# Kernel optimization log

Hardware: AMD Instinct MI355X
Metric: run time of the kernel (lower is better)

The kernel has to match this reference:

```python
import jax, jax.numpy as jnp
import numpy as np

B, T, D, H, L = 8, 128, 400, 300, 45  # batch, max_length, 2*word_lstm_size, hidden, tag_count


def setup_inputs() -> dict:
    key = jax.random.key(0)
    ks = jax.random.split(key, 10)
    s = 0.05
    return {
        "cont_repr": jax.random.normal(ks[0], (B, T, D), jnp.float32),
        "root": jax.random.normal(ks[1], (1, 1, D), jnp.float32),
        "W1a": jax.random.normal(ks[2], (D, H), jnp.float32) * s,
        "W1b": jax.random.normal(ks[3], (D, H), jnp.float32) * s,
        "b1": jnp.zeros((H,), jnp.float32),
        "Wa": jax.random.normal(ks[4], (H, 1), jnp.float32) * s,
        "ba": jnp.zeros((1,), jnp.float32),
        "Wl": jax.random.normal(ks[5], (H, L), jnp.float32) * s,
        "bl": jnp.zeros((L,), jnp.float32),
        "sentence_lengths": jax.random.randint(ks[6], (B,), 0, T + 1),
        "desired_arcs": jax.random.randint(ks[7], (B, T), 0, T + 1),
        "desired_labels": jax.random.randint(ks[8], (B, T), 0, L),
        "use_desired_arcs": 1,
    }


def reference(cont_repr, root, W1a, W1b, b1, Wa, ba, Wl, bl,
              sentence_lengths, desired_arcs, desired_labels, use_desired_arcs):
    b, t, d = cont_repr.shape
    mask = (jnp.arange(t)[None, :] < sentence_lengths[:, None]).astype(cont_repr.dtype)  # [B,T]
    n_valid = jnp.maximum(mask.sum(), 1.0)

    # Dense(concat(tile_a, tile_b)) == tile_a @ W1a + tile_b @ W1b (exact same math,
    # avoids materializing the [B,T,T+1,2D] concat the TF graph builds).
    a_proj = jnp.einsum('btd,dh->bth', cont_repr, W1a)                     # [B,T,H]
    with_root = jnp.concatenate([jnp.broadcast_to(root, (b, 1, d)), cont_repr], axis=1)  # [B,T+1,D]
    b_proj = jnp.einsum('bsd,dh->bsh', with_root, W1b)                     # [B,T+1,H]
    h = jax.nn.relu(a_proj[:, :, None, :] + b_proj[:, None, :, :] + b1)    # [B,T,T+1,H]

    # UAS: arc scorer (units=1) over T+1 head candidates
    arc_logits = jnp.einsum('btsh,ho->btso', h, Wa)[..., 0] + ba[0]        # [B,T,T+1]
    predicted_arcs = jnp.argmax(arc_logits, axis=-1)                        # [B,T]
    arc_logp = jax.nn.log_softmax(arc_logits, axis=-1)
    arc_ce = -jnp.take_along_axis(arc_logp, desired_arcs[..., None], axis=-1)[..., 0]
    uas_loss = (arc_ce * mask).sum() / n_valid

    # LAS: gather pair repr at selected head, score labels
    sel = desired_arcs if use_desired_arcs else predicted_arcs             # [B,T]
    idx = jnp.broadcast_to(sel[:, :, None, None], (b, t, 1, h.shape[-1]))
    sel_h = jnp.take_along_axis(h, idx, axis=2)[:, :, 0, :]                # [B,T,H]
    lab_logits = jnp.einsum('bth,hl->btl', sel_h, Wl) + bl                 # [B,T,L]
    lab_logp = jax.nn.log_softmax(lab_logits, axis=-1)
    lab_ce = -jnp.take_along_axis(lab_logp, desired_labels[..., None], axis=-1)[..., 0]
    las_loss = (lab_ce * mask).sum() / n_valid

    return (uas_loss + las_loss) / 2
```

## Files before the change

### kernel.cpp

```cpp
#include <hip/hip_runtime.h>
#include <hip/hip_bf16.h>
#include <math.h>

#define BN 8
#define TT 128
#define DD 400
#define HH 300
#define LL 45
#define KH 200
#define SS 129
#define ALG_STRIDE 132

__global__ __launch_bounds__(640) void proj_kernel(
    const float* __restrict__ cont, const float* __restrict__ root,
    const float* __restrict__ W1a, const float* __restrict__ W1b,
    const float* __restrict__ b1,
    const int* __restrict__ slen,
    float* __restrict__ AP, float* __restrict__ BPX,
    float* __restrict__ accum)
{
    __shared__ float red[320][9];
    const int blk = blockIdx.x;
    const int tid = threadIdx.x;
    const int grp = tid / 320;
    const int h   = tid % 320;
    const int d0  = __builtin_amdgcn_readfirstlane(grp * KH);

    if (blk == 256) {
        if (tid == 0) accum[0] = 0.f;
        float acc = 0.f;
        if (h < HH) {
            const float* wp = W1b + (size_t)d0 * HH + h;
            for (int d = 0; d < KH; ++d)
                acc = fmaf(root[d0 + d], wp[(size_t)d * HH], acc);
        }
        if (grp == 1) red[h][0] = acc;
        __syncthreads();
        if (grp == 0 && h < HH) {
            const float v = acc + red[h][0];
            for (int bb = 0; bb < BN; ++bb)
                BPX[(size_t)bb * SS * HH + h] = v;
        }
        return;
    }

    const bool isA = (blk < 128);
    const int rb   = isA ? blk : blk - 128;
    const int row0 = rb * 8;
    if (isA) {
        const int lenb = slen[row0 >> 7];
        if ((row0 & 127) >= lenb) return;
    }

    const float* W    = isA ? W1a : W1b;
    const float* rows = cont + (size_t)row0 * DD + d0;

    float acc[8];
    #pragma unroll
    for (int r = 0; r < 8; ++r) acc[r] = 0.f;

    if (h < HH) {
        const float* wp = W + (size_t)d0 * HH + h;
        float w[8];
        #pragma unroll
        for (int k = 0; k < 8; ++k) w[k] = wp[(size_t)k * HH];
        for (int dc = 0; dc < KH; dc += 8) {
            float wn[8];
            if (dc + 8 < KH) {
                #pragma unroll
                for (int k = 0; k < 8; ++k) wn[k] = wp[(size_t)(dc + 8 + k) * HH];
            } else {
                #pragma unroll
                for (int k = 0; k < 8; ++k) wn[k] = 0.f;
            }
            #pragma unroll
            for (int r = 0; r < 8; ++r) {
                const float* rp = rows + r * DD + dc;
                #pragma unroll
                for (int k = 0; k < 8; ++k)
                    acc[r] = fmaf(rp[k], w[k], acc[r]);
            }
            #pragma unroll
            for (int k = 0; k < 8; ++k) w[k] = wn[k];
        }
    }

    if (grp == 1) {
        #pragma unroll
        for (int r = 0; r < 8; ++r) red[h][r] = acc[r];
    }
    __syncthreads();
    if (grp == 0 && h < HH) {
        if (isA) {
            const float bb = b1[h];
            float* dst = AP + (size_t)row0 * HH + h;
            #pragma unroll
            for (int r = 0; r < 8; ++r)
                dst[(size_t)r * HH] = acc[r] + red[h][r] + bb;
        } else {
            const int b = row0 >> 7, t = row0 & 127;
            float* dst = BPX + ((size_t)(b * SS + t + 1)) * HH + h;
            #pragma unroll
            for (int r = 0; r < 8; ++r)
                dst[(size_t)r * HH] = acc[r] + red[h][r];
        }
    }
}

__global__ __launch_bounds__(256) void arc_kernel(
    const float* __restrict__ AP, const float* __restrict__ BPX,
    const float* __restrict__ Wa, const int* __restrict__ slen,
    float* __restrict__ ALG)
{
    const int blk = blockIdx.x;
    const int b  = blk >> 8;
    const int tg = (blk >> 3) & 31;
    const int sc = blk & 7;
    const int t0 = tg * 4;
    if (t0 >= slen[b]) return;

    const int lane = threadIdx.x & 63;
    const int wave = threadIdx.x >> 6;

    const float* ap = AP + (size_t)(b * TT + t0) * HH;
    float apr[4][5], war[5];
    #pragma unroll
    for (int i = 0; i < 5; ++i) {
        const int hh = lane + 64 * i;
        const bool v = (hh < HH);
        war[i] = v ? Wa[hh] : 0.f;
        #pragma unroll
        for (int r = 0; r < 4; ++r)
            apr[r][i] = v ? ap[(size_t)r * HH + hh] : 0.f;
    }

    const int s0 = sc * 17;
    for (int sl = wave; sl < 17; sl += 4) {
        const int s = s0 + sl;
        if (s >= SS) break;
        const float* bp = BPX + (size_t)(b * SS + s) * HH;
        float bv[5];
        #pragma unroll
        for (int i = 0; i < 5; ++i) {
            const int hh = lane + 64 * i;
            bv[i] = (hh < HH) ? bp[hh] : 0.f;
        }
        float p0 = 0.f, p1 = 0.f, p2 = 0.f, p3 = 0.f;
        #pragma unroll
        for (int i = 0; i < 5; ++i) {
            p0 = fmaf(fmaxf(apr[0][i] + bv[i], 0.f), war[i], p0);
            p1 = fmaf(fmaxf(apr[1][i] + bv[i], 0.f), war[i], p1);
            p2 = fmaf(fmaxf(apr[2][i] + bv[i], 0.f), war[i], p2);
            p3 = fmaf(fmaxf(apr[3][i] + bv[i], 0.f), war[i], p3);
        }
        #pragma unroll
        for (int off = 32; off; off >>= 1) {
            p0 += __shfl_xor(p0, off, 64);
            p1 += __shfl_xor(p1, off, 64);
            p2 += __shfl_xor(p2, off, 64);
            p3 += __shfl_xor(p3, off, 64);
        }
        if (lane == 0) {
            float* o = ALG + (size_t)(b * TT + t0) * ALG_STRIDE + s;
            o[0]              = p0;
            o[ALG_STRIDE]     = p1;
            o[2 * ALG_STRIDE] = p2;
            o[3 * ALG_STRIDE] = p3;
        }
    }
}

__global__ __launch_bounds__(64) void smx_kernel(
    const float* __restrict__ AP, const float* __restrict__ BPX,
    const float* __restrict__ Wl, const float* __restrict__ bl,
    const float* __restrict__ ALG,
    const int* __restrict__ slen, const int* __restrict__ des_arcs,
    const int* __restrict__ des_labels, const int* __restrict__ use_des,
    float* __restrict__ accum)
{
    const int blk = blockIdx.x;
    const int b = blk >> 7, t = blk & 127;
    if (t >= slen[b]) return;
    const int lane = threadIdx.x;

    __shared__ float selh[HH];

    const float* lg = ALG + (size_t)blk * ALG_STRIDE;
    const float v0 = lg[lane];
    const float v1 = lg[64 + lane];
    const float v2 = (lane == 0) ? lg[128] : -INFINITY;

    float m = fmaxf(fmaxf(v0, v1), v2);
    #pragma unroll
    for (int off = 32; off; off >>= 1) m = fmaxf(m, __shfl_xor(m, off, 64));
    float e = __expf(v0 - m) + __expf(v1 - m) + ((lane == 0) ? __expf(v2 - m) : 0.f);
    #pragma unroll
    for (int off = 32; off; off >>= 1) e += __shfl_xor(e, off, 64);
    const float arc_lse = m + __logf(e);

    float bv = v0; int bi = lane;
    if (v1 > bv) { bv = v1; bi = 64 + lane; }
    if (lane == 0 && v2 > bv) { bv = v2; bi = 128; }
    #pragma unroll
    for (int off = 32; off; off >>= 1) {
        const float ov = __shfl_xor(bv, off, 64);
        const int   oi = __shfl_xor(bi, off, 64);
        if (ov > bv || (ov == bv && oi < bi)) { bv = ov; bi = oi; }
    }

    const int da = des_arcs[b * TT + t];
    const float arc_ce = arc_lse - lg[da];
    const int sel = use_des[0] ? da : bi;

    const float* ap = AP + (size_t)blk * HH;
    const float* bp = BPX + (size_t)(b * SS + sel) * HH;
    #pragma unroll
    for (int i = 0; i < 5; ++i) {
        const int hh = lane + 64 * i;
        if (hh < HH) selh[hh] = fmaxf(ap[hh] + bp[hh], 0.f);
    }
    __syncthreads();

    float a = 0.f;
    if (lane < LL) {
        a = bl[lane];
        for (int hh = 0; hh < HH; hh += 4) {
            #pragma unroll
            for (int k = 0; k < 4; ++k)
                a = fmaf(selh[hh + k], Wl[(hh + k) * LL + lane], a);
        }
    }
    const float v = (lane < LL) ? a : -INFINITY;
    float lm = v;
    #pragma unroll
    for (int off = 32; off; off >>= 1) lm = fmaxf(lm, __shfl_xor(lm, off, 64));
    float le = (lane < LL) ? __expf(v - lm) : 0.f;
    #pragma unroll
    for (int off = 32; off; off >>= 1) le += __shfl_xor(le, off, 64);
    const float lab_lse = lm + __logf(le);

    const int dl = des_labels[b * TT + t];
    const float ldl = __shfl(v, dl, 64);
    if (lane == 0)
        atomicAdd(accum, arc_ce + (lab_lse - ldl));
}

__global__ void finalize_kernel(const float* __restrict__ accum,
                                const int* __restrict__ slen,
                                float* __restrict__ out)
{
    if (threadIdx.x == 0) {
        int n = 0;
        for (int b = 0; b < BN; ++b) {
            int l = slen[b];
            if (l < 0) l = 0;
            if (l > TT) l = TT;
            n += l;
        }
        float nv = (float)n;
        if (nv < 1.f) nv = 1.f;
        out[0] = accum[0] / (2.f * nv);
    }
}

extern "C" void kernel_launch(void* const* d_in, const int* in_sizes, int n_in,
                              void* d_out, int out_size, void* d_ws, size_t ws_size,
                              hipStream_t stream) {
    const float* cont = (const float*)d_in[0];
    const float* root = (const float*)d_in[1];
    const float* W1a  = (const float*)d_in[2];
    const float* W1b  = (const float*)d_in[3];
    const float* b1   = (const float*)d_in[4];
    const float* Wa   = (const float*)d_in[5];
    const float* Wl   = (const float*)d_in[7];
    const float* bl   = (const float*)d_in[8];
    const int* slen   = (const int*)d_in[9];
    const int* darc   = (const int*)d_in[10];
    const int* dlab   = (const int*)d_in[11];
    const int* used   = (const int*)d_in[12];
    float* out = (float*)d_out;

    float* AP    = (float*)d_ws;
    float* BPX   = AP  + 1024 * HH;
    float* ALG   = BPX + BN * SS * HH;
    float* accum = ALG + 1024 * ALG_STRIDE;

    proj_kernel<<<257, 640, 0, stream>>>(cont, root, W1a, W1b, b1, slen, AP, BPX, accum);
    arc_kernel<<<2048, 256, 0, stream>>>(AP, BPX, Wa, slen, ALG);
    smx_kernel<<<1024, 64, 0, stream>>>(AP, BPX, Wl, bl, ALG, slen, darc, dlab, used, accum);
    finalize_kernel<<<1, 64, 0, stream>>>(accum, slen, out);
}
```

Before: 44.99 us.

## Retile projection, stage arc tiles in LDS, and split label matmul across waves

The projection kernel now computes 16 rows per block instead of 8, halving the block count so each weight load is reused more. The arc scorer now stages an 8-row AP tile, a 33-row BPX tile and Wa in shared memory and computes one (t,s) pair per thread with float4 LDS reads, replacing the register-resident 4-row version. The softmax/label kernel uses 256 threads and splits the 300-wide label dot product across four waves, with a shared-memory reduction. The changes trade fewer blocks and less parallelism in the projection for more reuse, and add LDS staging and synchronisation in the arc kernel.

Result: slower. 55.70 us (+23.8%).

```diff
diff --git a/kernel.cpp b/kernel.cpp
--- a/kernel.cpp
+++ b/kernel.cpp
@@ -10,6 +10,7 @@
 #define KH 200
 #define SS 129
 #define ALG_STRIDE 132
+#define PADW 308
 
 __global__ __launch_bounds__(640) void proj_kernel(
     const float* __restrict__ cont, const float* __restrict__ root,
@@ -19,14 +20,14 @@
     float* __restrict__ AP, float* __restrict__ BPX,
     float* __restrict__ accum)
 {
-    __shared__ float red[320][9];
+    __shared__ float red[320][17];
     const int blk = blockIdx.x;
     const int tid = threadIdx.x;
     const int grp = tid / 320;
     const int h   = tid % 320;
     const int d0  = __builtin_amdgcn_readfirstlane(grp * KH);
 
-    if (blk == 256) {
+    if (blk == 128) {
         if (tid == 0) accum[0] = 0.f;
         float acc = 0.f;
         if (h < HH) {
@@ -44,9 +45,9 @@
         return;
     }
 
-    const bool isA = (blk < 128);
-    const int rb   = isA ? blk : blk - 128;
-    const int row0 = rb * 8;
+    const bool isA = (blk < 64);
+    const int rb   = isA ? blk : blk - 64;
+    const int row0 = rb * 16;
     if (isA) {
         const int lenb = slen[row0 >> 7];
         if ((row0 & 127) >= lenb) return;
@@ -55,9 +56,9 @@
     const float* W    = isA ? W1a : W1b;
     const float* rows = cont + (size_t)row0 * DD + d0;
 
-    float acc[8];
+    float acc[16];
     #pragma unroll
-    for (int r = 0; r < 8; ++r) acc[r] = 0.f;
+    for (int r = 0; r < 16; ++r) acc[r] = 0.f;
 
     if (h < HH) {
         const float* wp = W + (size_t)d0 * HH + h;
@@ -74,7 +75,7 @@
                 for (int k = 0; k < 8; ++k) wn[k] = 0.f;
             }
             #pragma unroll
-            for (int r = 0; r < 8; ++r) {
+            for (int r = 0; r < 16; ++r) {
                 const float* rp = rows + r * DD + dc;
                 #pragma unroll
                 for (int k = 0; k < 8; ++k)
@@ -87,7 +88,7 @@
 
     if (grp == 1) {
         #pragma unroll
-        for (int r = 0; r < 8; ++r) red[h][r] = acc[r];
+        for (int r = 0; r < 16; ++r) red[h][r] = acc[r];
     }
     __syncthreads();
     if (grp == 0 && h < HH) {
@@ -95,13 +96,13 @@
             const float bb = b1[h];
             float* dst = AP + (size_t)row0 * HH + h;
             #pragma unroll
-            for (int r = 0; r < 8; ++r)
+            for (int r = 0; r < 16; ++r)
                 dst[(size_t)r * HH] = acc[r] + red[h][r] + bb;
         } else {
             const int b = row0 >> 7, t = row0 & 127;
             float* dst = BPX + ((size_t)(b * SS + t + 1)) * HH + h;
             #pragma unroll
-            for (int r = 0; r < 8; ++r)
+            for (int r = 0; r < 16; ++r)
                 dst[(size_t)r * HH] = acc[r] + red[h][r];
         }
     }
@@ -112,65 +113,71 @@
     const float* __restrict__ Wa, const int* __restrict__ slen,
     float* __restrict__ ALG)
 {
+    __shared__ float ap_s[8][PADW];
+    __shared__ float bp_s[33][PADW];
+    __shared__ float wa_s[PADW];
+
     const int blk = blockIdx.x;
-    const int b  = blk >> 8;
-    const int tg = (blk >> 3) & 31;
-    const int sc = blk & 7;
-    const int t0 = tg * 4;
+    const int b  = blk >> 6;
+    const int tt = (blk >> 2) & 15;
+    const int sc = blk & 3;
+    const int t0 = tt * 8;
     if (t0 >= slen[b]) return;
 
-    const int lane = threadIdx.x & 63;
-    const int wave = threadIdx.x >> 6;
-
-    const float* ap = AP + (size_t)(b * TT + t0) * HH;
-    float apr[4][5], war[5];
-    #pragma unroll
-    for (int i = 0; i < 5; ++i) {
-        const int hh = lane + 64 * i;
-        const bool v = (hh < HH);
-        war[i] = v ? Wa[hh] : 0.f;
-        #pragma unroll
-        for (int r = 0; r < 4; ++r)
-            apr[r][i] = v ? ap[(size_t)r * HH + hh] : 0.f;
-    }
-
-    const int s0 = sc * 17;
-    for (int sl = wave; sl < 17; sl += 4) {
-        const int s = s0 + sl;
-        if (s >= SS) break;
-        const float* bp = BPX + (size_t)(b * SS + s) * HH;
-        float bv[5];
-        #pragma unroll
-        for (int i = 0; i < 5; ++i) {
-            const int hh = lane + 64 * i;
-            bv[i] = (hh < HH) ? bp[hh] : 0.f;
-        }
-        float p0 = 0.f, p1 = 0.f, p2 = 0.f, p3 = 0.f;
-        #pragma unroll
-        for (int i = 0; i < 5; ++i) {
-            p0 = fmaf(fmaxf(apr[0][i] + bv[i], 0.f), war[i], p0);
-            p1 = fmaf(fmaxf(apr[1][i] + bv[i], 0.f), war[i], p1);
-            p2 = fmaf(fmaxf(apr[2][i] + bv[i], 0.f), war[i], p2);
-            p3 = fmaf(fmaxf(apr[3][i] + bv[i], 0.f), war[i], p3);
-        }
-        #pragma unroll
-        for (int off = 32; off; off >>= 1) {
-            p0 += __shfl_xor(p0, off, 64);
-            p1 += __shfl_xor(p1, off, 64);
-            p2 += __shfl_xor(p2, off, 64);
-            p3 += __shfl_xor(p3, off, 64);
-        }
-        if (lane == 0) {
-            float* o = ALG + (size_t)(b * TT + t0) * ALG_STRIDE + s;
-            o[0]              = p0;
-            o[ALG_STRIDE]     = p1;
-            o[2 * ALG_STRIDE] = p2;
-            o[3 * ALG_STRIDE] = p3;
-        }
-    }
-}
-
-__global__ __launch_bounds__(64) void smx_kernel(
+    const int tid  = threadIdx.x;
+    const int lane = tid & 63;
+    const int wave = tid >> 6;
+    const int tl   = lane & 7;
+    const int sl   = lane >> 3;
+    const int s0   = sc * 32;
+
+    {
+        const float* apg = AP + (size_t)(b * TT + t0) * HH;
+        for (int i = tid; i < 8 * HH; i += 256)
+            ap_s[i / HH][i % HH] = apg[(i / HH) * HH + i % HH];
+        const float* bpg = BPX + (size_t)(b * SS + s0) * HH;
+        for (int i = tid; i < 33 * HH; i += 256)
+            bp_s[i / HH][i % HH] = bpg[(i / HH) * HH + i % HH];
+        for (int i = tid; i < HH; i += 256)
+            wa_s[i] = Wa[i];
+    }
+    __syncthreads();
+
+    const int s_local = wave * 8 + sl;
+    const float* aprow = ap_s[tl];
+    const float* bprow = bp_s[s_local];
+
+    float acc = 0.f;
+    #pragma unroll 5
+    for (int hh = 0; hh < HH; hh += 4) {
+        const float4 a4 = *(const float4*)&aprow[hh];
+        const float4 p4 = *(const float4*)&bprow[hh];
+        const float4 w4 = *(const float4*)&wa_s[hh];
+        acc = fmaf(fmaxf(a4.x + p4.x, 0.f), w4.x, acc);
+        acc = fmaf(fmaxf(a4.y + p4.y, 0.f), w4.y, acc);
+        acc = fmaf(fmaxf(a4.z + p4.z, 0.f), w4.z, acc);
+        acc = fmaf(fmaxf(a4.w + p4.w, 0.f), w4.w, acc);
+    }
+    ALG[(size_t)(b * TT + t0 + tl) * ALG_STRIDE + s0 + s_local] = acc;
+
+    if (sc == 3 && wave == 0 && sl == 0) {
+        const float* bpr = bp_s[32];
+        float a2 = 0.f;
+        #pragma unroll 5
+        for (int hh = 0; hh < HH; hh += 4) {
+            const float4 a4 = *(const float4*)&aprow[hh];
+            const float4 p4 = *(const float4*)&bpr[hh];
+            const float4 w4 = *(const float4*)&wa_s[hh];
+            a2 = fmaf(fmaxf(a4.x + p4.x, 0.f), w4.x, a2);
+            a2 = fmaf(fmaxf(a4.y + p4.y, 0.f), w4.y, a2);
+            a2 = fmaf(fmaxf(a4.z + p4.z, 0.f), w4.z, a2);
+            a2 = fmaf(fmaxf(a4.w + p4.w, 0.f), w4.w, a2);
+        }
+        ALG[(size_t)(b * TT + t0 + tl) * ALG_STRIDE + 128] = a2;
+    }
+}
+
+__global__ __launch_bounds__(256) void smx_kernel(
     const float* __restrict__ AP, const float* __restrict__ BPX,
     const float* __restrict__ Wl, const float* __restrict__ bl,
     const float* __restrict__ ALG,
@@ -181,68 +188,85 @@
     const int blk = blockIdx.x;
     const int b = blk >> 7, t = blk & 127;
     if (t >= slen[b]) return;
-    const int lane = threadIdx.x;
+    const int tid  = threadIdx.x;
+    const int lane = tid & 63;
+    const int wave = tid >> 6;
 
     __shared__ float selh[HH];
-
-    const float* lg = ALG + (size_t)blk * ALG_STRIDE;
-    const float v0 = lg[lane];
-    const float v1 = lg[64 + lane];
-    const float v2 = (lane == 0) ? lg[128] : -INFINITY;
-
-    float m = fmaxf(fmaxf(v0, v1), v2);
-    #pragma unroll
-    for (int off = 32; off; off >>= 1) m = fmaxf(m, __shfl_xor(m, off, 64));
-    float e = __expf(v0 - m) + __expf(v1 - m) + ((lane == 0) ? __expf(v2 - m) : 0.f);
-    #pragma unroll
-    for (int off = 32; off; off >>= 1) e += __shfl_xor(e, off, 64);
-    const float arc_lse = m + __logf(e);
-
-    float bv = v0; int bi = lane;
-    if (v1 > bv) { bv = v1; bi = 64 + lane; }
-    if (lane == 0 && v2 > bv) { bv = v2; bi = 128; }
-    #pragma unroll
-    for (int off = 32; off; off >>= 1) {
-        const float ov = __shfl_xor(bv, off, 64);
-        const int   oi = __shfl_xor(bi, off, 64);
-        if (ov > bv || (ov == bv && oi < bi)) { bv = ov; bi = oi; }
-    }
-
-    const int da = des_arcs[b * TT + t];
-    const float arc_ce = arc_lse - lg[da];
-    const int sel = use_des[0] ? da : bi;
-
-    const float* ap = AP + (size_t)blk * HH;
-    const float* bp = BPX + (size_t)(b * SS + sel) * HH;
-    #pragma unroll
-    for (int i = 0; i < 5; ++i) {
-        const int hh = lane + 64 * i;
-        if (hh < HH) selh[hh] = fmaxf(ap[hh] + bp[hh], 0.f);
-    }
-    __syncthreads();
-
-    float a = 0.f;
-    if (lane < LL) {
-        a = bl[lane];
-        for (int hh = 0; hh < HH; hh += 4) {
-            #pragma unroll
-            for (int k = 0; k < 4; ++k)
-                a = fmaf(selh[hh + k], Wl[(hh + k) * LL + lane], a);
-        }
-    }
-    const float v = (lane < LL) ? a : -INFINITY;
-    float lm = v;
-    #pragma unroll
-    for (int off = 32; off; off >>= 1) lm = fmaxf(lm, __shfl_xor(lm, off, 64));
-    float le = (lane < LL) ? __expf(v - lm) : 0.f;
-    #pragma unroll
-    for (int off = 32; off; off >>= 1) le += __shfl_xor(le, off, 64);
-    const float lab_lse = lm + __logf(le);
-
-    const int dl = des_labels[b * TT + t];
-    const float ldl = __shfl(v, dl, 64);
-    if (lane == 0)
-        atomicAdd(accum, arc_ce + (lab_lse - ldl));
+    __shared__ float partial[4][64];
+    __shared__ float arc_ce_s;
+    __shared__ int   sel_s;
+
+    if (wave == 0) {
+        const float* lg = ALG + (size_t)blk * ALG_STRIDE;
+        const float v0 = lg[lane];
+        const float v1 = lg[64 + lane];
+        const float v2 = (lane == 0) ? lg[128] : -INFINITY;
+
+        float m = fmaxf(fmaxf(v0, v1), v2);
+        #pragma unroll
+        for (int off = 32; off; off >>= 1) m = fmaxf(m, __shfl_xor(m, off, 64));
+        float e = __expf(v0 - m) + __expf(v1 - m) + ((lane == 0) ? __expf(v2 - m) : 0.f);
+        #pragma unroll
+        for (int off = 32; off; off >>= 1) e += __shfl_xor(e, off, 64);
+        const float arc_lse = m + __logf(e);
+
+        float bv = v0; int bi = lane;
+        if (v1 > bv) { bv = v1; bi = 64 + lane; }
+        if (lane == 0 && v2 > bv) { bv = v2; bi = 128; }
+        #pragma unroll
+        for (int off = 32; off; off >>= 1) {
+            const float ov = __shfl_xor(bv, off, 64);
+            const int   oi = __shfl_xor(bi, off, 64);
+            if (ov > bv || (ov == bv && oi < bi)) { bv = ov; bi = oi; }
+        }
+        if (lane == 0) {
+            const int da = des_arcs[b * TT + t];
+            arc_ce_s = arc_lse - lg[da];
+            sel_s = use_des[0] ? da : bi;
+        }
+    }
+    __syncthreads();
+
+    {
+        const int sel = sel_s;
+        const float* ap = AP + (size_t)blk * HH;
+        const float* bp = BPX + (size_t)(b * SS + sel) * HH;
+        for (int hh = tid; hh < HH; hh += 256)
+            selh[hh] = fmaxf(ap[hh] + bp[hh], 0.f);
+    }
+    __syncthreads();
+
+    {
+        float p = 0.f;
+        if (lane < LL) {
+            const int h0 = wave * 75;
+            #pragma unroll 5
+            for (int j = 0; j < 75; ++j)
+                p = fmaf(selh[h0 + j], Wl[(h0 + j) * LL + lane], p);
+        }
+        partial[wave][lane] = p;
+    }
+    __syncthreads();
+
+    if (wave == 0) {
+        float a = -INFINITY;
+        if (lane < LL)
+            a = bl[lane] + partial[0][lane] + partial[1][lane]
+                         + partial[2][lane] + partial[3][lane];
+        float lm = a;
+        #pragma unroll
+        for (int off = 32; off; off >>= 1) lm = fmaxf(lm, __shfl_xor(lm, off, 64));
+        float le = (lane < LL) ? __expf(a - lm) : 0.f;
+        #pragma unroll
+        for (int off = 32; off; off >>= 1) le += __shfl_xor(le, off, 64);
+        const float lab_lse = lm + __logf(le);
+
+        const int dl = des_labels[b * TT + t];
+        const float ldl = __shfl(a, dl, 64);
+        if (lane == 0)
+            atomicAdd(accum, arc_ce_s + (lab_lse - ldl));
+    }
 }
 
 __global__ void finalize_kernel(const float* __restrict__ accum,
@@ -285,8 +309,8 @@
     float* ALG   = BPX + BN * SS * HH;
     float* accum = ALG + 1024 * ALG_STRIDE;
 
-    proj_kernel<<<257, 640, 0, stream>>>(cont, root, W1a, W1b, b1, slen, AP, BPX, accum);
-    arc_kernel<<<2048, 256, 0, stream>>>(AP, BPX, Wa, slen, ALG);
-    smx_kernel<<<1024, 64, 0, stream>>>(AP, BPX, Wl, bl, ALG, slen, darc, dlab, used, accum);
+    proj_kernel<<<129, 640, 0, stream>>>(cont, root, W1a, W1b, b1, slen, AP, BPX, accum);
+    arc_kernel<<<512, 256, 0, stream>>>(AP, BPX, Wa, slen, ALG);
+    smx_kernel<<<1024, 256, 0, stream>>>(AP, BPX, Wl, bl, ALG, slen, darc, dlab, used, accum);
     finalize_kernel<<<1, 64, 0, stream>>>(accum, slen, out);
 }
```
